# Optimization experiments

Hardware: AMD Instinct MI355X
Metric: run time of the kernel (lower is better)

## Reference

```python
import jax, jax.numpy as jnp
import numpy as np

T, N, E = 12, 10000, 320000
IN_DIM, HID_DIM, EMB_DIM = 64, 128, 64


def setup_inputs() -> dict:
    key = jax.random.key(0)
    ks = jax.random.split(key, 12)
    s1 = 1.0 / np.sqrt(IN_DIM)
    s2 = 1.0 / np.sqrt(HID_DIM)
    sg = 1.0 / np.sqrt(EMB_DIM)
    return {
        "x_seq": jax.random.normal(ks[0], (T, N, IN_DIM), dtype=jnp.float32),
        "edge_index": jax.random.randint(ks[1], (2, E), 0, N, dtype=jnp.int64),
        "edge_weight": jax.random.uniform(ks[2], (E,), dtype=jnp.float32),
        # GCNConv layer 1 (weight stored as [in, out])
        "W1": jax.random.uniform(ks[3], (IN_DIM, HID_DIM), minval=-s1, maxval=s1, dtype=jnp.float32),
        "b1": jnp.zeros((HID_DIM,), dtype=jnp.float32),
        # GCNConv layer 2
        "W2": jax.random.uniform(ks[4], (HID_DIM, EMB_DIM), minval=-s2, maxval=s2, dtype=jnp.float32),
        "b2": jnp.zeros((EMB_DIM,), dtype=jnp.float32),
        # GRU params (torch layout: [3H, in] with gate order r, z, n)
        "W_ih": jax.random.uniform(ks[5], (3 * EMB_DIM, EMB_DIM), minval=-sg, maxval=sg, dtype=jnp.float32),
        "W_hh": jax.random.uniform(ks[6], (3 * EMB_DIM, EMB_DIM), minval=-sg, maxval=sg, dtype=jnp.float32),
        "b_ih": jax.random.uniform(ks[7], (3 * EMB_DIM,), minval=-sg, maxval=sg, dtype=jnp.float32),
        "b_hh": jax.random.uniform(ks[8], (3 * EMB_DIM,), minval=-sg, maxval=sg, dtype=jnp.float32),
        "dec_bias": jnp.zeros((1,), dtype=jnp.float32),
    }


def _gcn_conv(x, W, b, row, col, ew, n):
    # PyG GCNConv with self-loops already appended to (row, col, ew).
    deg = jax.ops.segment_sum(ew, col, num_segments=n)  # [N]
    dinv = jnp.where(deg > 0, jax.lax.rsqrt(jnp.where(deg > 0, deg, 1.0)), 0.0)
    norm = dinv[row] * ew * dinv[col]                   # [E+N]
    h = x @ W                                           # [N, out]
    agg = jax.ops.segment_sum(h[row] * norm[:, None], col, num_segments=n)
    return agg + b


def reference(x_seq, edge_index, edge_weight, W1, b1, W2, b2, W_ih, W_hh, b_ih, b_hh, dec_bias):
    n = x_seq.shape[1]
    loop = jnp.arange(n, dtype=edge_index.dtype)
    row = jnp.concatenate([edge_index[0], loop])
    col = jnp.concatenate([edge_index[1], loop])
    ew = jnp.concatenate([edge_weight, jnp.ones((n,), dtype=edge_weight.dtype)])

    def encode(x):  # x: [N, in_dim]
        h = jax.nn.relu(_gcn_conv(x, W1, b1, row, col, ew, n))
        # dropout p=0.3 only active in training; eval -> identity
        return _gcn_conv(h, W2, b2, row, col, ew, n)  # [N, emb]

    z_seq = jax.vmap(encode)(x_seq)  # [T, N, emb]

    emb = z_seq.shape[-1]

    def gru_step(h, xt):
        gi = xt @ W_ih.T + b_ih      # [N, 3H]
        gh = h @ W_hh.T + b_hh       # [N, 3H]
        i_r, i_z, i_n = jnp.split(gi, 3, axis=-1)
        h_r, h_z, h_n = jnp.split(gh, 3, axis=-1)
        r = jax.nn.sigmoid(i_r + h_r)
        zg = jax.nn.sigmoid(i_z + h_z)
        ng = jnp.tanh(i_n + r * h_n)
        h_new = (1.0 - zg) * ng + zg * h
        return h_new, None

    h0 = jnp.zeros((n, emb), dtype=x_seq.dtype)
    z, _ = jax.lax.scan(gru_step, h0, z_seq)  # out[-1] == final hidden state

    od_pred = jax.nn.softplus(z @ z.T + dec_bias)  # [N, N]
    return od_pred, z
```

## Files before the change

### kernel.cpp

```cpp
#include <hip/hip_runtime.h>
#include <cstdint>
#include <cstddef>

#define T_STEPS 12
#define NNODES  10000
#define NEDGES  320000
#define IN_DIM  64
#define HID     128
#define EMB     64
#define G3      192
#define NPAD    10112

typedef __attribute__((ext_vector_type(8))) short short8;
typedef __attribute__((ext_vector_type(4))) float f32x4;

__global__ void k_setup(float* __restrict__ deg, int* __restrict__ cnt) {
    int i = blockIdx.x * 256 + threadIdx.x;
    if (i < NNODES) { deg[i] = 1.0f; cnt[i] = 1; }
}

__global__ void k_edge(const int* __restrict__ eidx, const float* __restrict__ ew,
                       float* __restrict__ deg, int* __restrict__ cnt) {
    int e = blockIdx.x * 256 + threadIdx.x;
    if (e >= NEDGES) return;
    int c = eidx[NEDGES + e];
    atomicAdd(&deg[c], ew[e]);
    atomicAdd(&cnt[c], 1);
}

__global__ void k_dinv(const float* __restrict__ deg, float* __restrict__ dinv) {
    int i = blockIdx.x * 256 + threadIdx.x;
    if (i >= NNODES) return;
    float d = deg[i];
    dinv[i] = (d > 0.0f) ? rsqrtf(d) : 0.0f;
}

__global__ __launch_bounds__(1024) void k_scan(const int* __restrict__ cnt,
                                               int* __restrict__ offs, int* __restrict__ cursor) {
    __shared__ int sh[1024];
    int t = threadIdx.x;
    int loc[10];
    int run = 0;
#pragma unroll
    for (int i = 0; i < 10; ++i) {
        int idx = t * 10 + i;
        int v = (idx < NNODES) ? cnt[idx] : 0;
        loc[i] = run;
        run += v;
    }
    sh[t] = run;
    __syncthreads();
    for (int off = 1; off < 1024; off <<= 1) {
        int v = 0;
        if (t >= off) v = sh[t - off];
        __syncthreads();
        if (t >= off) sh[t] += v;
        __syncthreads();
    }
    int base = (t > 0) ? sh[t - 1] : 0;
#pragma unroll
    for (int i = 0; i < 10; ++i) {
        int idx = t * 10 + i;
        if (idx < NNODES) {
            int e = base + loc[i];
            offs[idx] = e;
            cursor[idx] = e;
        }
    }
    if (t == 1023) offs[NNODES] = sh[1023];
}

__global__ void k_scatter(const int* __restrict__ eidx, const float* __restrict__ ew,
                          const float* __restrict__ dinv, int* __restrict__ cursor,
                          int2* __restrict__ edata) {
    int e = blockIdx.x * 256 + threadIdx.x;
    if (e < NEDGES) {
        int r = eidx[e];
        int c = eidx[NEDGES + e];
        float w = dinv[r] * ew[e] * dinv[c];
        int p = atomicAdd(&cursor[c], 1);
        edata[p] = make_int2(r, __float_as_int(w));
    } else if (e < NEDGES + NNODES) {
        int i = e - NEDGES;
        float di = dinv[i];
        int p = atomicAdd(&cursor[i], 1);
        edata[p] = make_int2(i, __float_as_int(di * di));
    }
}

template <int K, int NO, int GR, int RPT, bool BT, bool BIAS, bool RELU>
__global__ __launch_bounds__(NO* GR) void k_mm(const float* __restrict__ A,
                                               const float* __restrict__ B,
                                               const float* __restrict__ bias,
                                               float* __restrict__ C, int M) {
    constexpr int NOP = NO + 1;
    __shared__ float Bs[K * NOP];
    const int tid = threadIdx.x;
    constexpr int NTHR = NO * GR;
    for (int i = tid; i < K * NO; i += NTHR) {
        if (BT) { int k = i / NO, c = i - k * NO; Bs[k * NOP + c] = B[i]; }
        else    { int c = i / K,  k = i - c * K;  Bs[k * NOP + c] = B[i]; }
    }
    __syncthreads();
    const int c  = tid % NO;
    const int rg = tid / NO;
    const float bv = BIAS ? bias[c] : 0.0f;
    for (int r0 = (blockIdx.x * GR + rg) * RPT; r0 < M; r0 += gridDim.x * GR * RPT) {
        int r0u = __builtin_amdgcn_readfirstlane(r0);
        float acc[RPT];
#pragma unroll
        for (int i = 0; i < RPT; ++i) acc[i] = bv;
        const float4* A4 = (const float4*)A + (size_t)r0u * (K / 4);
        for (int k0 = 0; k0 < K; k0 += 4) {
            float a[RPT][4];
#pragma unroll
            for (int i = 0; i < RPT; ++i) {
                float4 v = A4[i * (K / 4) + (k0 >> 2)];
                a[i][0] = v.x; a[i][1] = v.y; a[i][2] = v.z; a[i][3] = v.w;
            }
#pragma unroll
            for (int j = 0; j < 4; ++j) {
                float b = Bs[(k0 + j) * NOP + c];
#pragma unroll
                for (int i = 0; i < RPT; ++i) acc[i] = fmaf(a[i][j], b, acc[i]);
            }
        }
#pragma unroll
        for (int i = 0; i < RPT; ++i) {
            float v = acc[i];
            if (RELU) v = fmaxf(v, 0.0f);
            C[(size_t)(r0 + i) * NO + c] = v;
        }
    }
}

template <bool BIAS>
__global__ __launch_bounds__(256) void k_aggt(const float* __restrict__ H,
                                              const int2* __restrict__ edata,
                                              const int* __restrict__ offs,
                                              const float* __restrict__ bias,
                                              float* __restrict__ out) {
    int node = (blockIdx.x * 256 + threadIdx.x) >> 6;
    node = __builtin_amdgcn_readfirstlane(node);
    if (node >= NNODES) return;
    int t = blockIdx.y;
    int lane = threadIdx.x & 63;
    const float* Ht = H + (size_t)t * (NNODES * EMB);
    int beg = offs[node], end = offs[node + 1];
    float acc = BIAS ? bias[lane] : 0.0f;
    for (int e0 = beg; e0 < end; e0 += 64) {
        int idx = e0 + lane;
        int2 ed = (idx < end) ? edata[idx] : make_int2(0, 0);
        int sv = ed.x;
        float wv = __int_as_float(ed.y);
        int m = min(64, end - e0);
#pragma unroll 4
        for (int j = 0; j < m; ++j) {
            int sj = __shfl(sv, j);
            float wj = __shfl(wv, j);
            acc = fmaf(wj, Ht[sj * EMB + lane], acc);
        }
    }
    out[(size_t)t * (NNODES * EMB) + (size_t)node * EMB + lane] = acc;
}

__global__ __launch_bounds__(192, 3) void k_gru(const float* __restrict__ gi,
                                                const float* __restrict__ W_hh,
                                                const float* __restrict__ b_hh,
                                                float* __restrict__ hout) {
    constexpr int RPB = 6;
    __shared__ float ghs[RPB][G3 + 1];
    __shared__ float hs[RPB][64];
    int tid = threadIdx.x;
    float wv[64];
    const float4* W4 = (const float4*)(W_hh + (size_t)tid * 64);
#pragma unroll
    for (int j = 0; j < 16; ++j) {
        float4 v = W4[j];
        wv[4 * j + 0] = v.x; wv[4 * j + 1] = v.y;
        wv[4 * j + 2] = v.z; wv[4 * j + 3] = v.w;
    }
    for (int i = tid; i < RPB * 64; i += 192) ((float*)hs)[i] = 0.0f;
    __syncthreads();
    int r0 = blockIdx.x * RPB;
    float bh = b_hh[tid];
    for (int t = 0; t < T_STEPS; ++t) {
        float acc[RPB];
#pragma unroll
        for (int i = 0; i < RPB; ++i) acc[i] = bh;
#pragma unroll
        for (int k0 = 0; k0 < 64; k0 += 4) {
#pragma unroll
            for (int i = 0; i < RPB; ++i) {
                float4 h4 = *(const float4*)&hs[i][k0];
                acc[i] = fmaf(h4.x, wv[k0 + 0], acc[i]);
                acc[i] = fmaf(h4.y, wv[k0 + 1], acc[i]);
                acc[i] = fmaf(h4.z, wv[k0 + 2], acc[i]);
                acc[i] = fmaf(h4.w, wv[k0 + 3], acc[i]);
            }
        }
#pragma unroll
        for (int i = 0; i < RPB; ++i) ghs[i][tid] = acc[i];
        __syncthreads();
#pragma unroll
        for (int it = 0; it < 2; ++it) {
            int item = it * 192 + tid;
            int rr = item >> 6, f = item & 63;
            int grow = r0 + rr;
            if (grow < NNODES) {
                const float* gir = gi + ((size_t)t * NNODES + grow) * G3;
                float ir = gir[f], iz = gir[64 + f], inn = gir[128 + f];
                float hr = ghs[rr][f], hz = ghs[rr][64 + f], hn = ghs[rr][128 + f];
                float rg = 1.0f / (1.0f + expf(-(ir + hr)));
                float zg = 1.0f / (1.0f + expf(-(iz + hz)));
                float ng = tanhf(fmaf(rg, hn, inn));
                float hp = hs[rr][f];
                hs[rr][f] = fmaf(zg, hp - ng, ng);
            }
        }
        __syncthreads();
    }
#pragma unroll
    for (int it = 0; it < 2; ++it) {
        int item = it * 192 + tid;
        int rr = item >> 6, f = item & 63;
        int grow = r0 + rr;
        if (grow < NNODES) hout[(size_t)grow * 64 + f] = hs[rr][f];
    }
}

__global__ void k_zcopy(const float* __restrict__ h, float* __restrict__ out) {
    int i = blockIdx.x * 256 + threadIdx.x;
    if (i < NNODES * EMB) out[(size_t)NNODES * NNODES + i] = h[i];
}

__global__ void k_zsplit(const float* __restrict__ h,
                         unsigned short* __restrict__ zhi, unsigned short* __restrict__ zlo) {
    int i = blockIdx.x * 256 + threadIdx.x;
    if (i >= NPAD * EMB) return;
    float x = (i < NNODES * EMB) ? h[i] : 0.0f;
    uint32_t b = __float_as_uint(x);
    uint32_t rh = (b + 0x7FFFu + ((b >> 16) & 1u)) & 0xFFFF0000u;
    float fhi = __uint_as_float(rh);
    float lo = x - fhi;
    uint32_t bl = __float_as_uint(lo);
    uint32_t rl = (bl + 0x7FFFu + ((bl >> 16) & 1u)) & 0xFFFF0000u;
    zhi[i] = (unsigned short)(rh >> 16);
    zlo[i] = (unsigned short)(rl >> 16);
}

__device__ __forceinline__ float softplus_fast(float x) {
    float e = __builtin_amdgcn_exp2f(-1.4426950408889634f * fabsf(x));
    float l = 0.6931471805599453f * __builtin_amdgcn_logf(1.0f + e);
    return fmaxf(x, 0.0f) + l;
}

__global__ __launch_bounds__(256) void k_dec(const unsigned short* __restrict__ zhi,
                                             const unsigned short* __restrict__ zlo,
                                             const float* __restrict__ dbias,
                                             float* __restrict__ out) {
    union DecSmem {
        struct { short A[128 * 128]; short B[128 * 128]; } ab;
        float C[128 * 128];
    };
    __shared__ DecSmem sm;
    int tid = threadIdx.x;
    int r0 = blockIdx.y * 128, c0 = blockIdx.x * 128;
    const float4* zh4 = (const float4*)zhi;
    const float4* zl4 = (const float4*)zlo;
#pragma unroll
    for (int p8 = 0; p8 < 8; ++p8) {
        int idx = p8 * 256 + tid;
        int row = idx >> 4, c = idx & 15;
        float4 va = (c < 8) ? zh4[(size_t)(r0 + row) * 8 + c] : zl4[(size_t)(r0 + row) * 8 + (c - 8)];
        float4 vb = (c < 8) ? zh4[(size_t)(c0 + row) * 8 + c] : zl4[(size_t)(c0 + row) * 8 + (c - 8)];
        int pos = c ^ (row & 15);
        *(float4*)&sm.ab.A[row * 128 + pos * 8] = va;
        *(float4*)&sm.ab.B[row * 128 + pos * 8] = vb;
    }
    __syncthreads();
    int lane = tid & 63, w = tid >> 6;
    int r = lane & 15, q = lane >> 4;
    f32x4 acc[2][8];
#pragma unroll
    for (int mt = 0; mt < 2; ++mt)
#pragma unroll
        for (int nt = 0; nt < 8; ++nt) acc[mt][nt] = (f32x4){0.f, 0.f, 0.f, 0.f};
    const int aSel[6] = {0, 4, 0, 4, 8, 12};
    const int bSel[6] = {0, 4, 8, 12, 0, 4};
#pragma unroll
    for (int ks = 0; ks < 6; ++ks) {
        short8 af[2], bf[8];
#pragma unroll
        for (int mt = 0; mt < 2; ++mt) {
            int rowA = w * 32 + mt * 16 + r;
            af[mt] = *(const short8*)&sm.ab.A[rowA * 128 + ((aSel[ks] + q) ^ r) * 8];
        }
#pragma unroll
        for (int nt = 0; nt < 8; ++nt) {
            int rowB = nt * 16 + r;
            bf[nt] = *(const short8*)&sm.ab.B[rowB * 128 + ((bSel[ks] + q) ^ r) * 8];
        }
#pragma unroll
        for (int mt = 0; mt < 2; ++mt)
#pragma unroll
            for (int nt = 0; nt < 8; ++nt)
                acc[mt][nt] = __builtin_amdgcn_mfma_f32_16x16x32_bf16(af[mt], bf[nt], acc[mt][nt], 0, 0, 0);
    }
    float db = dbias[0];
    __syncthreads();
#pragma unroll
    for (int mt = 0; mt < 2; ++mt) {
        int rowb = w * 32 + mt * 16 + q * 4;
#pragma unroll
        for (int nt = 0; nt < 8; ++nt) {
            int col = nt * 16 + r;
#pragma unroll
            for (int reg = 0; reg < 4; ++reg) {
                int row = rowb + reg;
                sm.C[row * 128 + (col ^ ((row & 4) << 2))] = softplus_fast(acc[mt][nt][reg] + db);
            }
        }
    }
    __syncthreads();
    bool full = (r0 + 128 <= NNODES) && (c0 + 128 <= NNODES);
    if (full) {
#pragma unroll
        for (int p = 0; p < 16; ++p) {
            int idx = p * 256 + tid;
            int row = idx >> 5, k = idx & 31;
            float4 v = *(const float4*)&sm.C[row * 128 + ((k * 4) ^ ((row & 4) << 2))];
            *(float4*)&out[(size_t)(r0 + row) * NNODES + c0 + k * 4] = v;
        }
    } else {
        for (int p = 0; p < 16; ++p) {
            int idx = p * 256 + tid;
            int row = idx >> 5, k = idx & 31;
            int gr = r0 + row;
            int gc = c0 + k * 4;
            if (gr >= NNODES || gc >= NNODES) continue;
            float4 v = *(const float4*)&sm.C[row * 128 + ((k * 4) ^ ((row & 4) << 2))];
            if (gc + 4 <= NNODES) {
                *(float4*)&out[(size_t)gr * NNODES + gc] = v;
            } else {
                float vv[4] = {v.x, v.y, v.z, v.w};
                for (int j = 0; j < 4 && gc + j < NNODES; ++j)
                    out[(size_t)gr * NNODES + gc + j] = vv[j];
            }
        }
    }
}

extern "C" void kernel_launch(void* const* d_in, const int* in_sizes, int n_in,
                              void* d_out, int out_size, void* d_ws, size_t ws_size,
                              hipStream_t stream) {
    const float* x_seq = (const float*)d_in[0];
    const int*   eidx  = (const int*)d_in[1];
    const float* ew    = (const float*)d_in[2];
    const float* W1    = (const float*)d_in[3];
    const float* b1    = (const float*)d_in[4];
    const float* W2    = (const float*)d_in[5];
    const float* b2    = (const float*)d_in[6];
    const float* W_ih  = (const float*)d_in[7];
    const float* W_hh  = (const float*)d_in[8];
    const float* b_ih  = (const float*)d_in[9];
    const float* b_hh  = (const float*)d_in[10];
    const float* dbias = (const float*)d_in[11];
    float* out = (float*)d_out;

    char* wsp = (char*)d_ws;
    auto alloc = [&](size_t bytes) {
        char* p = wsp;
        wsp += (bytes + 255) & ~(size_t)255;
        return p;
    };
    float* deg    = (float*)alloc((size_t)NNODES * 4);
    float* dinv   = (float*)alloc((size_t)NNODES * 4);
    int*   cnt    = (int*)alloc((size_t)NNODES * 4);
    int*   offs   = (int*)alloc((size_t)(NNODES + 1) * 4);
    int*   cursor = (int*)alloc((size_t)NNODES * 4);
    int2*  edata  = (int2*)alloc((size_t)(NEDGES + NNODES) * 8);
    float* hst    = (float*)alloc((size_t)NNODES * EMB * 4);
    unsigned short* zhi = (unsigned short*)alloc((size_t)NPAD * EMB * 2);
    unsigned short* zlo = (unsigned short*)alloc((size_t)NPAD * EMB * 2);
    float* Buf1   = (float*)alloc((size_t)T_STEPS * NNODES * G3 * 4);
    float* Buf2   = (float*)alloc((size_t)T_STEPS * NNODES * HID * 4);

    const int M = T_STEPS * NNODES;
    float* xa = Buf2;
    float* g2 = Buf2 + (size_t)T_STEPS * NNODES * EMB;
    float* z  = Buf2;
    float* h1 = Buf1;
    float* gi = Buf1;

    k_setup<<<(NNODES + 255) / 256, 256, 0, stream>>>(deg, cnt);
    k_edge<<<(NEDGES + 255) / 256, 256, 0, stream>>>(eidx, ew, deg, cnt);
    k_dinv<<<(NNODES + 255) / 256, 256, 0, stream>>>(deg, dinv);
    k_scan<<<1, 1024, 0, stream>>>(cnt, offs, cursor);
    k_scatter<<<(NEDGES + NNODES + 255) / 256, 256, 0, stream>>>(eidx, ew, dinv, cursor, edata);

    dim3 gagg((NNODES * 64 + 255) / 256, T_STEPS);
    k_aggt<false><<<gagg, 256, 0, stream>>>(x_seq, edata, offs, nullptr, xa);
    k_mm<64, 128, 2, 8, true, true, true><<<1024, 256, 0, stream>>>(xa, W1, b1, h1, M);
    k_mm<128, 64, 4, 8, true, false, false><<<1024, 256, 0, stream>>>(h1, W2, nullptr, g2, M);
    k_aggt<true><<<gagg, 256, 0, stream>>>(g2, edata, offs, b2, z);
    k_mm<64, 192, 1, 8, false, true, false><<<1024, 192, 0, stream>>>(z, W_ih, b_ih, gi, M);
    k_gru<<<(NNODES + 5) / 6, 192, 0, stream>>>(gi, W_hh, b_hh, hst);
    k_zcopy<<<(NNODES * EMB + 255) / 256, 256, 0, stream>>>(hst, out);
    k_zsplit<<<(NPAD * EMB + 255) / 256, 256, 0, stream>>>(hst, zhi, zlo);
    dim3 gdec(NPAD / 128, NPAD / 128);
    k_dec<<<gdec, 256, 0, stream>>>(zhi, zlo, dbias, out);
}
```

Before: 1.210 ms.

## Aggregate two timesteps per wavefront, write GRU state directly to output, nontemporal stores

The edge aggregation kernel now handles two timesteps per wavefront, so each CSR edge record and its shuffles are reused for two feature gathers and the grid's time dimension is halved. The GRU writes its final hidden state straight into the z region of the output buffer, which removes the separate copy kernel. Nontemporal loads and stores are used for edge data, aggregation outputs and the large decoder output to reduce cache pollution. Halving the grid lowers parallelism in the aggregation kernel and raises register use per thread.

Measured after the change: 1.129 ms. 1.07x faster.

```diff
diff --git a/kernel.cpp b/kernel.cpp
--- a/kernel.cpp
+++ b/kernel.cpp
@@ -143,25 +143,31 @@
     int node = (blockIdx.x * 256 + threadIdx.x) >> 6;
     node = __builtin_amdgcn_readfirstlane(node);
     if (node >= NNODES) return;
-    int t = blockIdx.y;
+    int t0 = blockIdx.y * 2;
     int lane = threadIdx.x & 63;
-    const float* Ht = H + (size_t)t * (NNODES * EMB);
+    const float* H0 = H + (size_t)t0 * (NNODES * EMB);
+    const float* H1 = H0 + (size_t)(NNODES * EMB);
     int beg = offs[node], end = offs[node + 1];
-    float acc = BIAS ? bias[lane] : 0.0f;
+    float bv = BIAS ? bias[lane] : 0.0f;
+    float acc0 = bv, acc1 = bv;
     for (int e0 = beg; e0 < end; e0 += 64) {
         int idx = e0 + lane;
-        int2 ed = (idx < end) ? edata[idx] : make_int2(0, 0);
-        int sv = ed.x;
-        float wv = __int_as_float(ed.y);
+        unsigned long long ev = (idx < end)
+            ? __builtin_nontemporal_load((const unsigned long long*)&edata[idx]) : 0ull;
+        int sv = (int)(ev & 0xFFFFFFFFull);
+        float wv = __int_as_float((int)(ev >> 32));
         int m = min(64, end - e0);
 #pragma unroll 4
         for (int j = 0; j < m; ++j) {
             int sj = __shfl(sv, j);
             float wj = __shfl(wv, j);
-            acc = fmaf(wj, Ht[sj * EMB + lane], acc);
-        }
-    }
-    out[(size_t)t * (NNODES * EMB) + (size_t)node * EMB + lane] = acc;
+            acc0 = fmaf(wj, H0[sj * EMB + lane], acc0);
+            acc1 = fmaf(wj, H1[sj * EMB + lane], acc1);
+        }
+    }
+    size_t o0 = (size_t)t0 * (NNODES * EMB) + (size_t)node * EMB + lane;
+    __builtin_nontemporal_store(acc0, &out[o0]);
+    __builtin_nontemporal_store(acc1, &out[o0 + (size_t)(NNODES * EMB)]);
 }
 
 __global__ __launch_bounds__(192, 3) void k_gru(const float* __restrict__ gi,
@@ -229,11 +235,6 @@
     }
 }
 
-__global__ void k_zcopy(const float* __restrict__ h, float* __restrict__ out) {
-    int i = blockIdx.x * 256 + threadIdx.x;
-    if (i < NNODES * EMB) out[(size_t)NNODES * NNODES + i] = h[i];
-}
-
 __global__ void k_zsplit(const float* __restrict__ h,
                          unsigned short* __restrict__ zhi, unsigned short* __restrict__ zlo) {
     int i = blockIdx.x * 256 + threadIdx.x;
@@ -329,8 +330,8 @@
         for (int p = 0; p < 16; ++p) {
             int idx = p * 256 + tid;
             int row = idx >> 5, k = idx & 31;
-            float4 v = *(const float4*)&sm.C[row * 128 + ((k * 4) ^ ((row & 4) << 2))];
-            *(float4*)&out[(size_t)(r0 + row) * NNODES + c0 + k * 4] = v;
+            f32x4 v = *(const f32x4*)&sm.C[row * 128 + ((k * 4) ^ ((row & 4) << 2))];
+            __builtin_nontemporal_store(v, (f32x4*)&out[(size_t)(r0 + row) * NNODES + c0 + k * 4]);
         }
     } else {
         for (int p = 0; p < 16; ++p) {
@@ -380,7 +381,6 @@
     int*   offs   = (int*)alloc((size_t)(NNODES + 1) * 4);
     int*   cursor = (int*)alloc((size_t)NNODES * 4);
     int2*  edata  = (int2*)alloc((size_t)(NEDGES + NNODES) * 8);
-    float* hst    = (float*)alloc((size_t)NNODES * EMB * 4);
     unsigned short* zhi = (unsigned short*)alloc((size_t)NPAD * EMB * 2);
     unsigned short* zlo = (unsigned short*)alloc((size_t)NPAD * EMB * 2);
     float* Buf1   = (float*)alloc((size_t)T_STEPS * NNODES * G3 * 4);
@@ -392,6 +392,7 @@
     float* z  = Buf2;
     float* h1 = Buf1;
     float* gi = Buf1;
+    float* hst = out + (size_t)NNODES * NNODES;
 
     k_setup<<<(NNODES + 255) / 256, 256, 0, stream>>>(deg, cnt);
     k_edge<<<(NEDGES + 255) / 256, 256, 0, stream>>>(eidx, ew, deg, cnt);
@@ -399,14 +400,13 @@
     k_scan<<<1, 1024, 0, stream>>>(cnt, offs, cursor);
     k_scatter<<<(NEDGES + NNODES + 255) / 256, 256, 0, stream>>>(eidx, ew, dinv, cursor, edata);
 
-    dim3 gagg((NNODES * 64 + 255) / 256, T_STEPS);
+    dim3 gagg((NNODES * 64 + 255) / 256, T_STEPS / 2);
     k_aggt<false><<<gagg, 256, 0, stream>>>(x_seq, edata, offs, nullptr, xa);
     k_mm<64, 128, 2, 8, true, true, true><<<1024, 256, 0, stream>>>(xa, W1, b1, h1, M);
     k_mm<128, 64, 4, 8, true, false, false><<<1024, 256, 0, stream>>>(h1, W2, nullptr, g2, M);
     k_aggt<true><<<gagg, 256, 0, stream>>>(g2, edata, offs, b2, z);
     k_mm<64, 192, 1, 8, false, true, false><<<1024, 192, 0, stream>>>(z, W_ih, b_ih, gi, M);
     k_gru<<<(NNODES + 5) / 6, 192, 0, stream>>>(gi, W_hh, b_hh, hst);
-    k_zcopy<<<(NNODES * EMB + 255) / 256, 256, 0, stream>>>(hst, out);
     k_zsplit<<<(NPAD * EMB + 255) / 256, 256, 0, stream>>>(hst, zhi, zlo);
     dim3 gdec(NPAD / 128, NPAD / 128);
     k_dec<<<gdec, 256, 0, stream>>>(zhi, zlo, dbias, out);
```
